# Kernel optimization log

Measured on AMD Instinct MI355X. Metric: run time of the kernel, lower is better.

Reference implementation:

```python
import jax, jax.numpy as jnp
import numpy as np

B = 32768; NF = 8; E = 16; V = 100000; D = 4
IN = 2 * NF * E          # 256 = id_dims + agn_dims
FCN = [256, 128, 64]
DIMS = [IN] + FCN
EPS = 1e-5               # BatchNorm1d eps


def setup_inputs() -> dict:
    ks = jax.random.split(jax.random.key(0), 64)
    inp = {
        'id_idx': jax.random.randint(ks[0], (B, NF), 0, V),
        'agn_idx': jax.random.randint(ks[1], (B, NF), 0, V),
        'domain_id': jax.random.randint(ks[2], (B,), 0, D),
        'id_tables': jax.random.normal(ks[3], (NF, V, E), dtype=jnp.float32) * 0.01,
        'agn_tables': jax.random.normal(ks[4], (NF, V, E), dtype=jnp.float32) * 0.01,
    }
    k = 5
    for i in range(len(FCN)):
        din, dout = DIMS[i], DIMS[i + 1]
        inp[f'mlp_W{i}'] = jax.random.normal(ks[k], (D, din, dout), dtype=jnp.float32) / np.sqrt(din).astype(np.float32); k += 1
        inp[f'mlp_b{i}'] = jnp.zeros((D, dout), jnp.float32)
        inp[f'bn_g{i}'] = jnp.ones((D, dout), jnp.float32)
        inp[f'bn_b{i}'] = jnp.zeros((D, dout), jnp.float32)
        inp[f'gate_W1_{i}'] = jax.random.normal(ks[k], (D, IN, dout), dtype=jnp.float32) / np.sqrt(IN).astype(np.float32); k += 1
        inp[f'gate_b1_{i}'] = jnp.zeros((D, dout), jnp.float32)
        inp[f'gate_W2_{i}'] = jax.random.normal(ks[k], (D, dout, dout), dtype=jnp.float32) / np.sqrt(dout).astype(np.float32); k += 1
        inp[f'gate_b2_{i}'] = jnp.zeros((D, dout), jnp.float32)
    inp['fin_W'] = jax.random.normal(ks[k], (D, DIMS[-1], 1), dtype=jnp.float32) / np.sqrt(DIMS[-1]).astype(np.float32)
    inp['fin_b'] = jnp.zeros((D, 1), jnp.float32)
    return inp


def _embed(tables, idx):
    # tables [NF,V,E], idx [B,NF] -> [B, NF*E] (per-feature lookup then concat)
    g = tables[jnp.arange(NF)[None, :], idx]            # [B,NF,E]
    return g.reshape(idx.shape[0], NF * E)


def _ppnet(id_tables, agn_tables, mlp_W, mlp_b, bn_g, bn_b, gW1, gb1, gW2, gb2,
           fin_W, fin_b, id_idx, agn_idx, domain_id):
    id_x = _embed(id_tables, id_idx)                    # [B, 128]
    agn_x = _embed(agn_tables, agn_idx)                 # [B, 128]
    # gate_input = cat(id_x, agn_x.detach())
    gate_in = jnp.concatenate([id_x, jax.lax.stop_gradient(agn_x)], axis=1)  # [B, IN]
    h = None
    for i in range(len(FCN)):
        # GateNU: Linear->ReLU->Linear->2*sigmoid, broadcast over D domain towers
        g1 = jax.nn.relu(jnp.einsum('bi,dio->dbo', gate_in, gW1[i]) + gb1[i][:, None, :])
        gate = 2.0 * jax.nn.sigmoid(jnp.einsum('dbo,dop->dbp', g1, gW2[i]) + gb2[i][:, None, :])
        # MLP layer: Linear -> BatchNorm1d (train-mode batch stats) -> ReLU
        if h is None:
            h = jnp.einsum('bi,dio->dbo', gate_in, mlp_W[i]) + mlp_b[i][:, None, :]
        else:
            h = jnp.einsum('dbi,dio->dbo', h, mlp_W[i]) + mlp_b[i][:, None, :]
        mu = h.mean(axis=1, keepdims=True)
        var = h.var(axis=1, keepdims=True)              # biased, matches torch BN training
        h = (h - mu) * jax.lax.rsqrt(var + EPS) * bn_g[i][:, None, :] + bn_b[i][:, None, :]
        h = jax.nn.relu(h)
        h = h * gate
    out = jax.nn.sigmoid(jnp.einsum('dbh,dho->dbo', h, fin_W) + fin_b[:, None, :])  # [D,B,1]
    out = out[:, :, 0]                                  # [D,B]
    # torch.where masked-select chain == gather the row of the assigned domain
    return out[domain_id, jnp.arange(out.shape[1])]     # [B]


def reference(id_idx, agn_idx, domain_id, id_tables, agn_tables,
              mlp_W0, mlp_b0, bn_g0, bn_b0, gate_W1_0, gate_b1_0, gate_W2_0, gate_b2_0,
              mlp_W1, mlp_b1, bn_g1, bn_b1, gate_W1_1, gate_b1_1, gate_W2_1, gate_b2_1,
              mlp_W2, mlp_b2, bn_g2, bn_b2, gate_W1_2, gate_b1_2, gate_W2_2, gate_b2_2,
              fin_W, fin_b):
    mlp_W = [mlp_W0, mlp_W1, mlp_W2]; mlp_b = [mlp_b0, mlp_b1, mlp_b2]
    bn_g = [bn_g0, bn_g1, bn_g2]; bn_b = [bn_b0, bn_b1, bn_b2]
    gW1 = [gate_W1_0, gate_W1_1, gate_W1_2]; gb1 = [gate_b1_0, gate_b1_1, gate_b1_2]
    gW2 = [gate_W2_0, gate_W2_1, gate_W2_2]; gb2 = [gate_b2_0, gate_b2_1, gate_b2_2]
    return _ppnet(id_tables, agn_tables, mlp_W, mlp_b, bn_g, bn_b, gW1, gb1, gW2, gb2,
                  fin_W, fin_b, id_idx, agn_idx, domain_id)
```

## Files before the change

### kernel.cpp

```cpp
#include <hip/hip_runtime.h>


typedef __attribute__((ext_vector_type(8))) short short8;
typedef __attribute__((ext_vector_type(4))) float floatx4;

#define BATCH 32768
#define NDOM 4
#define TM 64

__device__ __forceinline__ unsigned short f2b(float f) {
    unsigned u = __float_as_uint(f);
    u += 0x7fffu + ((u >> 16) & 1u);
    return (unsigned short)(u >> 16);
}
__device__ __forceinline__ float b2f(unsigned short h) {
    return __uint_as_float(((unsigned)h) << 16);
}

struct MatDesc { const float* src; unsigned K, N, pfx, total; };
struct PrepArgs { MatDesc m[9]; float* stats; unsigned statsN; unsigned grand; };

__global__ __launch_bounds__(256) void prep_k(PrepArgs a, unsigned short* __restrict__ wt) {
    unsigned e = blockIdx.x * 256 + threadIdx.x;
    if (e < a.statsN) a.stats[e] = 0.f;
    if (e >= a.grand) return;
    int j = 0;
    while (j < 8 && e >= a.m[j].pfx + a.m[j].total) j++;
    const unsigned K = a.m[j].K, N = a.m[j].N;
    const unsigned local = e - a.m[j].pfx;
    const unsigned kn = K * N;
    const unsigned d = local / kn;
    const unsigned r2 = local - d * kn;
    const unsigned n = r2 / K;
    const unsigned k = r2 - n * K;
    wt[e] = f2b(a.m[j].src[((long long)d * K + k) * N + n]);
}

__global__ __launch_bounds__(256) void embed_k(const int* __restrict__ idi, const int* __restrict__ agi,
                                               const float* __restrict__ idt, const float* __restrict__ agt,
                                               unsigned short* __restrict__ gin) {
    int t = blockIdx.x * 256 + threadIdx.x;
    int b = t >> 4, slot = t & 15;
    int f = slot & 7;
    const int* ip = (slot < 8) ? idi : agi;
    const float* tab = (slot < 8) ? idt : agt;
    int ix = ip[b * 8 + f];
    const float* src = tab + ((long long)f * 100000 + ix) * 16;
    unsigned short tmp[16];
#pragma unroll
    for (int j = 0; j < 16; j++) tmp[j] = f2b(src[j]);
    unsigned short* dst = gin + (long long)b * 256 + slot * 16;
    *(uint4*)dst = *(const uint4*)tmp;
    *(uint4*)(dst + 8) = *(const uint4*)(tmp + 8);
}

template <int N, int KX>
__global__ __launch_bounds__(256, 2) void stats_k(
    const unsigned short* __restrict__ X, int ginMode,
    const unsigned short* __restrict__ Wm,
    float* __restrict__ gsum, float* __restrict__ gssq) {
    constexpr int GX = KX / 8;
    constexpr int NW = N / 4, CT = NW / 16;
    __shared__ __align__(16) unsigned short tA[TM * KX];
    const int t = threadIdx.x;
    const int d = blockIdx.y;
    const int m0 = blockIdx.x * TM;
    const unsigned short* Xp = X + ((long long)(ginMode ? 0 : d * BATCH) + m0) * KX;
#pragma unroll
    for (int r = 0; r < TM * GX / 256; r++) {
        int idx = r * 256 + t;
        int m = idx / GX, j = idx % GX;
        uint4 v = *(const uint4*)(Xp + (long long)m * KX + j * 8);
        *(uint4*)&tA[(m * GX + (j ^ (m & 7))) * 8] = v;
    }
    __syncthreads();
    const int w = t >> 6, lane = t & 63, lrow = lane & 15, lq = lane >> 4;
    const int n0w = w * NW;
    const unsigned short* Wp = Wm + ((long long)d * N + n0w) * KX;
    floatx4 acc[4][CT];
#pragma unroll
    for (int rt = 0; rt < 4; rt++)
#pragma unroll
        for (int ct = 0; ct < CT; ct++) acc[rt][ct] = (floatx4)(0.f);
#pragma unroll
    for (int k0 = 0; k0 < KX; k0 += 32) {
        short8 a[4], b[CT];
#pragma unroll
        for (int rt = 0; rt < 4; rt++) {
            int m = rt * 16 + lrow;
            a[rt] = *(const short8*)&tA[(m * GX + (((k0 >> 3) | lq) ^ (m & 7))) * 8];
        }
#pragma unroll
        for (int ct = 0; ct < CT; ct++)
            b[ct] = *(const short8*)(Wp + (long long)(ct * 16 + lrow) * KX + k0 + lq * 8);
#pragma unroll
        for (int rt = 0; rt < 4; rt++)
#pragma unroll
            for (int ct = 0; ct < CT; ct++)
                acc[rt][ct] = __builtin_amdgcn_mfma_f32_16x16x32_bf16(a[rt], b[ct], acc[rt][ct], 0, 0, 0);
    }
#pragma unroll
    for (int ct = 0; ct < CT; ct++) {
        float s = 0.f, ss = 0.f;
#pragma unroll
        for (int rt = 0; rt < 4; rt++)
#pragma unroll
            for (int r = 0; r < 4; r++) { float v = acc[rt][ct][r]; s += v; ss += v * v; }
        s += __shfl_down(s, 32); ss += __shfl_down(ss, 32);
        s += __shfl_down(s, 16); ss += __shfl_down(ss, 16);
        if (lane < 16) {
            atomicAdd(&gsum[d * N + n0w + ct * 16 + lane], s);
            atomicAdd(&gssq[d * N + n0w + ct * 16 + lane], ss);
        }
    }
}

template <int N, int KX, bool SHARED_A, bool FINAL>
__global__ __launch_bounds__(256, 2) void fused_k(
    const unsigned short* __restrict__ gin,
    const unsigned short* __restrict__ Xh,
    const unsigned short* __restrict__ W1,
    const unsigned short* __restrict__ W2,
    const unsigned short* __restrict__ Wm,
    const float* __restrict__ gb1, const float* __restrict__ gb2,
    const float* __restrict__ gsum, const float* __restrict__ gssq,
    const float* __restrict__ gma, const float* __restrict__ bta, float invB,
    unsigned short* __restrict__ Xn,
    const int* __restrict__ dom, const float* __restrict__ fw,
    const float* __restrict__ fb, float* __restrict__ outp) {
    constexpr int GG = N / 8;
    constexpr int GX = KX / 8;
    constexpr int NW = N / 4, CT = NW / 16;
    constexpr int TXN = SHARED_A ? 8 : TM * KX;
    __shared__ __align__(16) unsigned short tG[TM * 256];
    __shared__ __align__(16) unsigned short tX[TXN];
    __shared__ __align__(16) unsigned short g1b[TM * N];
    const int t = threadIdx.x;
    const int d = blockIdx.y;
    const int m0 = blockIdx.x * TM;
    const int w = t >> 6, lane = t & 63, lrow = lane & 15, lq = lane >> 4;
    const int n0w = w * NW;

    {
        const unsigned short* Gp = gin + (long long)m0 * 256;
#pragma unroll
        for (int r = 0; r < 8; r++) {
            int idx = r * 256 + t;
            int m = idx >> 5, j = idx & 31;
            uint4 v = *(const uint4*)(Gp + (long long)m * 256 + j * 8);
            *(uint4*)&tG[((m << 5) + (j ^ (m & 7))) * 8] = v;
        }
    }
    if constexpr (!SHARED_A) {
        const unsigned short* Xp = Xh + ((long long)d * BATCH + m0) * KX;
#pragma unroll
        for (int r = 0; r < TM * GX / 256; r++) {
            int idx = r * 256 + t;
            int m = idx / GX, j = idx % GX;
            uint4 v = *(const uint4*)(Xp + (long long)m * KX + j * 8);
            *(uint4*)&tX[(m * GX + (j ^ (m & 7))) * 8] = v;
        }
    }
    __syncthreads();

    floatx4 acc1[4][CT], acch[4][CT];
#pragma unroll
    for (int rt = 0; rt < 4; rt++)
#pragma unroll
        for (int ct = 0; ct < CT; ct++) { acc1[rt][ct] = (floatx4)(0.f); acch[rt][ct] = (floatx4)(0.f); }
    const unsigned short* W1p = W1 + ((long long)d * N + n0w) * 256;
    const unsigned short* Wmp = Wm + ((long long)d * N + n0w) * KX;
#pragma unroll
    for (int k0 = 0; k0 < 256; k0 += 32) {
        short8 aG[4];
#pragma unroll
        for (int rt = 0; rt < 4; rt++) {
            int m = rt * 16 + lrow;
            aG[rt] = *(const short8*)&tG[((m << 5) + (((k0 >> 3) | lq) ^ (m & 7))) * 8];
        }
        short8 b1[CT];
#pragma unroll
        for (int ct = 0; ct < CT; ct++)
            b1[ct] = *(const short8*)(W1p + (long long)(ct * 16 + lrow) * 256 + k0 + lq * 8);
        if (k0 < KX) {
            short8 aX[4], bm[CT];
            if constexpr (SHARED_A) {
#pragma unroll
                for (int rt = 0; rt < 4; rt++) aX[rt] = aG[rt];
            } else {
#pragma unroll
                for (int rt = 0; rt < 4; rt++) {
                    int m = rt * 16 + lrow;
                    aX[rt] = *(const short8*)&tX[(m * GX + (((k0 >> 3) | lq) ^ (m & 7))) * 8];
                }
            }
#pragma unroll
            for (int ct = 0; ct < CT; ct++)
                bm[ct] = *(const short8*)(Wmp + (long long)(ct * 16 + lrow) * KX + k0 + lq * 8);
#pragma unroll
            for (int rt = 0; rt < 4; rt++)
#pragma unroll
                for (int ct = 0; ct < CT; ct++) {
                    acc1[rt][ct] = __builtin_amdgcn_mfma_f32_16x16x32_bf16(aG[rt], b1[ct], acc1[rt][ct], 0, 0, 0);
                    acch[rt][ct] = __builtin_amdgcn_mfma_f32_16x16x32_bf16(aX[rt], bm[ct], acch[rt][ct], 0, 0, 0);
                }
        } else {
#pragma unroll
            for (int rt = 0; rt < 4; rt++)
#pragma unroll
                for (int ct = 0; ct < CT; ct++)
                    acc1[rt][ct] = __builtin_amdgcn_mfma_f32_16x16x32_bf16(aG[rt], b1[ct], acc1[rt][ct], 0, 0, 0);
        }
    }
#pragma unroll
    for (int ct = 0; ct < CT; ct++) {
        int n = n0w + ct * 16 + lrow;
        float bs = gb1[d * N + n];
        int jj = n >> 3, sub = n & 7;
#pragma unroll
        for (int rt = 0; rt < 4; rt++)
#pragma unroll
            for (int r = 0; r < 4; r++) {
                int m = rt * 16 + lq * 4 + r;
                g1b[(m * GG + (jj ^ (m & 7))) * 8 + sub] = f2b(fmaxf(acc1[rt][ct][r] + bs, 0.f));
            }
    }
    __syncthreads();

    floatx4 acc2[4][CT];
#pragma unroll
    for (int rt = 0; rt < 4; rt++)
#pragma unroll
        for (int ct = 0; ct < CT; ct++) acc2[rt][ct] = (floatx4)(0.f);
    const unsigned short* W2p = W2 + ((long long)d * N + n0w) * N;
#pragma unroll
    for (int k0 = 0; k0 < N; k0 += 32) {
        short8 a[4], b[CT];
#pragma unroll
        for (int rt = 0; rt < 4; rt++) {
            int m = rt * 16 + lrow;
            a[rt] = *(const short8*)&g1b[(m * GG + (((k0 >> 3) | lq) ^ (m & 7))) * 8];
        }
#pragma unroll
        for (int ct = 0; ct < CT; ct++)
            b[ct] = *(const short8*)(W2p + (long long)(ct * 16 + lrow) * N + k0 + lq * 8);
#pragma unroll
        for (int rt = 0; rt < 4; rt++)
#pragma unroll
            for (int ct = 0; ct < CT; ct++)
                acc2[rt][ct] = __builtin_amdgcn_mfma_f32_16x16x32_bf16(a[rt], b[ct], acc2[rt][ct], 0, 0, 0);
    }
    __syncthreads();

#pragma unroll
    for (int ct = 0; ct < CT; ct++) {
        int n = n0w + ct * 16 + lrow;
        int i = d * N + n;
        float bs2 = gb2[i];
        float ma = gsum[i] * invB;
        float var = gssq[i] * invB - ma * ma;
        float sc = rsqrtf(var + 1e-5f) * gma[i];
        float sh = bta[i] - ma * sc;
        int jj = n >> 3, sub = n & 7;
#pragma unroll
        for (int rt = 0; rt < 4; rt++)
#pragma unroll
            for (int r = 0; r < 4; r++) {
                int m = rt * 16 + lq * 4 + r;
                float gate = 2.f / (1.f + __expf(-(acc2[rt][ct][r] + bs2)));
                float v = fmaxf(acch[rt][ct][r] * sc + sh, 0.f) * gate;
                g1b[(m * GG + (jj ^ (m & 7))) * 8 + sub] = f2b(v);
            }
    }
    __syncthreads();

    if (!FINAL) {
        unsigned short* Op = Xn + ((long long)d * BATCH + m0) * N;
#pragma unroll
        for (int r = 0; r < TM * GG / 256; r++) {
            int idx = r * 256 + t;
            int m = idx / GG, j = idx % GG;
            *(uint4*)(Op + (long long)m * N + j * 8) = *(const uint4*)&g1b[(m * GG + (j ^ (m & 7))) * 8];
        }
    } else {
        int m = t >> 2, q = t & 3;
        const float* fwp = fw + d * 64;
        float s = 0.f;
#pragma unroll
        for (int g = 0; g < 2; g++) {
            int j = q * 2 + g;
            short8 v = *(const short8*)&g1b[(m * 8 + (j ^ (m & 7))) * 8];
#pragma unroll
            for (int kk = 0; kk < 8; kk++)
                s += b2f((unsigned short)v[kk]) * fwp[j * 8 + kk];
        }
        s += __shfl_down(s, 1);
        s += __shfl_down(s, 2);
        if (q == 0) {
            int b = m0 + m;
            if (dom[b] == d) outp[b] = 1.f / (1.f + __expf(-(s + fb[d])));
        }
    }
}

extern "C" void kernel_launch(void* const* d_in, const int* in_sizes, int n_in,
                              void* d_out, int out_size, void* d_ws, size_t ws_size,
                              hipStream_t stream) {
    const int B = BATCH, D = NDOM;

    const int* id_idx = (const int*)d_in[0];
    const int* agn_idx = (const int*)d_in[1];
    const int* dom = (const int*)d_in[2];
    const float* id_t = (const float*)d_in[3];
    const float* agn_t = (const float*)d_in[4];
    const float *mlpW[3], *bng[3], *bnb[3], *gW1[3], *gb1[3], *gW2[3], *gb2[3];
    for (int i = 0; i < 3; i++) {
        int b0 = 5 + i * 8;
        mlpW[i] = (const float*)d_in[b0 + 0];
        bng[i] = (const float*)d_in[b0 + 2];
        bnb[i] = (const float*)d_in[b0 + 3];
        gW1[i] = (const float*)d_in[b0 + 4];
        gb1[i] = (const float*)d_in[b0 + 5];
        gW2[i] = (const float*)d_in[b0 + 6];
        gb2[i] = (const float*)d_in[b0 + 7];
    }
    const float* finW = (const float*)d_in[29];
    const float* finb = (const float*)d_in[30];

    char* wsc = (char*)d_ws;
    size_t off = 0;
    auto alloc = [&](size_t bytes) -> char* {
        char* p = wsc + off;
        off = (off + bytes + 255) & ~(size_t)255;
        return p;
    };

    struct { const float* src; int K, N; } mats[9] = {
        {mlpW[0], 256, 256}, {gW1[0], 256, 256}, {gW2[0], 256, 256},
        {mlpW[1], 256, 128}, {gW1[1], 256, 128}, {gW2[1], 128, 128},
        {mlpW[2], 128, 64},  {gW1[2], 256, 64},  {gW2[2], 64, 64}};
    unsigned pfx[10];
    pfx[0] = 0;
    for (int j = 0; j < 9; j++) pfx[j + 1] = pfx[j] + 4u * mats[j].K * mats[j].N;

    unsigned short* wt = (unsigned short*)alloc((size_t)pfx[9] * 2);
    unsigned short* gin = (unsigned short*)alloc((size_t)B * 256 * 2);
    float* stats = (float*)alloc((size_t)3 * 2 * D * 256 * 4);
    unsigned short* X1 = (unsigned short*)alloc((size_t)D * B * 256 * 2);
    unsigned short* X2 = (unsigned short*)alloc((size_t)D * B * 128 * 2);

    PrepArgs pa;
    for (int j = 0; j < 9; j++) {
        pa.m[j].src = mats[j].src;
        pa.m[j].K = (unsigned)mats[j].K;
        pa.m[j].N = (unsigned)mats[j].N;
        pa.m[j].pfx = pfx[j];
        pa.m[j].total = 4u * mats[j].K * mats[j].N;
    }
    pa.stats = stats;
    pa.statsN = 3 * 2 * D * 256;
    pa.grand = pfx[9];

    const float invB = 1.f / (float)B;
    dim3 gs(B / TM, D);

    prep_k<<<dim3((pfx[9] + 255) / 256), 256, 0, stream>>>(pa, wt);
    embed_k<<<dim3(B * 16 / 256), 256, 0, stream>>>(id_idx, agn_idx, id_t, agn_t, gin);

    float* gsum0 = stats + 0 * 2 * D * 256; float* gssq0 = gsum0 + D * 256;
    float* gsum1 = stats + 1 * 2 * D * 256; float* gssq1 = gsum1 + D * 256;
    float* gsum2 = stats + 2 * 2 * D * 256; float* gssq2 = gsum2 + D * 256;

    stats_k<256, 256><<<gs, 256, 0, stream>>>(gin, 1, wt + pfx[0], gsum0, gssq0);
    fused_k<256, 256, true, false><<<gs, 256, 0, stream>>>(
        gin, gin, wt + pfx[1], wt + pfx[2], wt + pfx[0], gb1[0], gb2[0],
        gsum0, gssq0, bng[0], bnb[0], invB,
        X1, nullptr, nullptr, nullptr, nullptr);

    stats_k<128, 256><<<gs, 256, 0, stream>>>(X1, 0, wt + pfx[3], gsum1, gssq1);
    fused_k<128, 256, false, false><<<gs, 256, 0, stream>>>(
        gin, X1, wt + pfx[4], wt + pfx[5], wt + pfx[3], gb1[1], gb2[1],
        gsum1, gssq1, bng[1], bnb[1], invB,
        X2, nullptr, nullptr, nullptr, nullptr);

    stats_k<64, 128><<<gs, 256, 0, stream>>>(X2, 0, wt + pfx[6], gsum2, gssq2);
    fused_k<64, 128, false, true><<<gs, 256, 0, stream>>>(
        gin, X2, wt + pfx[7], wt + pfx[8], wt + pfx[6], gb1[2], gb2[2],
        gsum2, gssq2, bng[2], bnb[2], invB,
        nullptr, dom, finW, finb, (float*)d_out);
}
```

Measured before the change: 535.2 us.

## Store pre-BN layer outputs and fuse next-layer matmul with stats into layer kernel

The separate stats kernels are removed, along with the recomputation of the pre-BN main-path matmul in the fused kernel. h0_k computes the first pre-BN activations, accumulates their BN statistics and writes them to memory. Each fused2_k then applies gating and BN to the stored h, computes the next layer's pre-BN matmul, accumulates its statistics and stores it. This cuts the kernel count from seven to five and drops the duplicate GEMMs. The cost is writing and reading bf16 pre-BN tensors through global memory, and shared memory is reused as a single buffer with extra barriers.

```diff
diff --git a/kernel.cpp b/kernel.cpp
--- a/kernel.cpp
+++ b/kernel.cpp
@@ -54,53 +54,52 @@
     *(uint4*)(dst + 8) = *(const uint4*)(tmp + 8);
 }
 
-template <int N, int KX>
-__global__ __launch_bounds__(256, 2) void stats_k(
-    const unsigned short* __restrict__ X, int ginMode,
+__global__ __launch_bounds__(256, 2) void h0_k(
+    const unsigned short* __restrict__ gin,
     const unsigned short* __restrict__ Wm,
-    float* __restrict__ gsum, float* __restrict__ gssq) {
-    constexpr int GX = KX / 8;
-    constexpr int NW = N / 4, CT = NW / 16;
-    __shared__ __align__(16) unsigned short tA[TM * KX];
+    float* __restrict__ gsum, float* __restrict__ gssq,
+    unsigned short* __restrict__ hOut) {
+    __shared__ __align__(16) unsigned short tA[TM * 256];
     const int t = threadIdx.x;
     const int d = blockIdx.y;
     const int m0 = blockIdx.x * TM;
-    const unsigned short* Xp = X + ((long long)(ginMode ? 0 : d * BATCH) + m0) * KX;
-#pragma unroll
-    for (int r = 0; r < TM * GX / 256; r++) {
+    const unsigned short* Xp = gin + (long long)m0 * 256;
+#pragma unroll
+    for (int r = 0; r < 8; r++) {
         int idx = r * 256 + t;
-        int m = idx / GX, j = idx % GX;
-        uint4 v = *(const uint4*)(Xp + (long long)m * KX + j * 8);
-        *(uint4*)&tA[(m * GX + (j ^ (m & 7))) * 8] = v;
+        int m = idx >> 5, j = idx & 31;
+        uint4 v = *(const uint4*)(Xp + (long long)m * 256 + j * 8);
+        *(uint4*)&tA[((m << 5) + (j ^ (m & 7))) * 8] = v;
     }
     __syncthreads();
     const int w = t >> 6, lane = t & 63, lrow = lane & 15, lq = lane >> 4;
-    const int n0w = w * NW;
-    const unsigned short* Wp = Wm + ((long long)d * N + n0w) * KX;
-    floatx4 acc[4][CT];
+    const int n0w = w * 64;
+    const unsigned short* Wp = Wm + ((long long)d * 256 + n0w) * 256;
+    floatx4 acc[4][4];
 #pragma unroll
     for (int rt = 0; rt < 4; rt++)
 #pragma unroll
-        for (int ct = 0; ct < CT; ct++) acc[rt][ct] = (floatx4)(0.f);
-#pragma unroll
-    for (int k0 = 0; k0 < KX; k0 += 32) {
-        short8 a[4], b[CT];
+        for (int ct = 0; ct < 4; ct++) acc[rt][ct] = (floatx4)(0.f);
+#pragma unroll
+    for (int k0 = 0; k0 < 256; k0 += 32) {
+        short8 a[4], b[4];
 #pragma unroll
         for (int rt = 0; rt < 4; rt++) {
             int m = rt * 16 + lrow;
-            a[rt] = *(const short8*)&tA[(m * GX + (((k0 >> 3) | lq) ^ (m & 7))) * 8];
-        }
-#pragma unroll
-        for (int ct = 0; ct < CT; ct++)
-            b[ct] = *(const short8*)(Wp + (long long)(ct * 16 + lrow) * KX + k0 + lq * 8);
-#pragma unroll
-        for (int rt = 0; rt < 4; rt++)
-#pragma unroll
-            for (int ct = 0; ct < CT; ct++)
+            a[rt] = *(const short8*)&tA[((m << 5) + (((k0 >> 3) | lq) ^ (m & 7))) * 8];
+        }
+#pragma unroll
+        for (int ct = 0; ct < 4; ct++)
+            b[ct] = *(const short8*)(Wp + (long long)(ct * 16 + lrow) * 256 + k0 + lq * 8);
+#pragma unroll
+        for (int rt = 0; rt < 4; rt++)
+#pragma unroll
+            for (int ct = 0; ct < 4; ct++)
                 acc[rt][ct] = __builtin_amdgcn_mfma_f32_16x16x32_bf16(a[rt], b[ct], acc[rt][ct], 0, 0, 0);
     }
-#pragma unroll
-    for (int ct = 0; ct < CT; ct++) {
+    __syncthreads();
+#pragma unroll
+    for (int ct = 0; ct < 4; ct++) {
         float s = 0.f, ss = 0.f;
 #pragma unroll
         for (int rt = 0; rt < 4; rt++)
@@ -109,32 +108,48 @@
         s += __shfl_down(s, 32); ss += __shfl_down(ss, 32);
         s += __shfl_down(s, 16); ss += __shfl_down(ss, 16);
         if (lane < 16) {
-            atomicAdd(&gsum[d * N + n0w + ct * 16 + lane], s);
-            atomicAdd(&gssq[d * N + n0w + ct * 16 + lane], ss);
-        }
-    }
-}
-
-template <int N, int KX, bool SHARED_A, bool FINAL>
-__global__ __launch_bounds__(256, 2) void fused_k(
+            atomicAdd(&gsum[d * 256 + n0w + ct * 16 + lane], s);
+            atomicAdd(&gssq[d * 256 + n0w + ct * 16 + lane], ss);
+        }
+        int n = n0w + ct * 16 + lrow;
+        int jj = n >> 3, sub = n & 7;
+#pragma unroll
+        for (int rt = 0; rt < 4; rt++)
+#pragma unroll
+            for (int r = 0; r < 4; r++) {
+                int m = rt * 16 + lq * 4 + r;
+                tA[((m << 5) + (jj ^ (m & 7))) * 8 + sub] = f2b(acc[rt][ct][r]);
+            }
+    }
+    __syncthreads();
+    unsigned short* Op = hOut + ((long long)d * BATCH + m0) * 256;
+#pragma unroll
+    for (int r = 0; r < 8; r++) {
+        int idx = r * 256 + t;
+        int m = idx >> 5, j = idx & 31;
+        *(uint4*)(Op + (long long)m * 256 + j * 8) = *(const uint4*)&tA[((m << 5) + (j ^ (m & 7))) * 8];
+    }
+}
+
+template <int N, int NH, bool FINAL>
+__global__ __launch_bounds__(256, 2) void fused2_k(
     const unsigned short* __restrict__ gin,
-    const unsigned short* __restrict__ Xh,
+    const unsigned short* __restrict__ hIn,
     const unsigned short* __restrict__ W1,
     const unsigned short* __restrict__ W2,
-    const unsigned short* __restrict__ Wm,
+    const unsigned short* __restrict__ WmN,
     const float* __restrict__ gb1, const float* __restrict__ gb2,
     const float* __restrict__ gsum, const float* __restrict__ gssq,
     const float* __restrict__ gma, const float* __restrict__ bta, float invB,
-    unsigned short* __restrict__ Xn,
+    unsigned short* __restrict__ hNext,
+    float* __restrict__ gsumN, float* __restrict__ gssqN,
     const int* __restrict__ dom, const float* __restrict__ fw,
     const float* __restrict__ fb, float* __restrict__ outp) {
     constexpr int GG = N / 8;
-    constexpr int GX = KX / 8;
     constexpr int NW = N / 4, CT = NW / 16;
-    constexpr int TXN = SHARED_A ? 8 : TM * KX;
-    __shared__ __align__(16) unsigned short tG[TM * 256];
-    __shared__ __align__(16) unsigned short tX[TXN];
-    __shared__ __align__(16) unsigned short g1b[TM * N];
+    constexpr int NWH = NH / 4, CTH = NH / 64;
+    constexpr int GH = NH / 8;
+    __shared__ __align__(16) unsigned short buf[TM * 256];
     const int t = threadIdx.x;
     const int d = blockIdx.y;
     const int m0 = blockIdx.x * TM;
@@ -148,70 +163,36 @@
             int idx = r * 256 + t;
             int m = idx >> 5, j = idx & 31;
             uint4 v = *(const uint4*)(Gp + (long long)m * 256 + j * 8);
-            *(uint4*)&tG[((m << 5) + (j ^ (m & 7))) * 8] = v;
-        }
-    }
-    if constexpr (!SHARED_A) {
-        const unsigned short* Xp = Xh + ((long long)d * BATCH + m0) * KX;
-#pragma unroll
-        for (int r = 0; r < TM * GX / 256; r++) {
-            int idx = r * 256 + t;
-            int m = idx / GX, j = idx % GX;
-            uint4 v = *(const uint4*)(Xp + (long long)m * KX + j * 8);
-            *(uint4*)&tX[(m * GX + (j ^ (m & 7))) * 8] = v;
-        }
-    }
-    __syncthreads();
-
-    floatx4 acc1[4][CT], acch[4][CT];
+            *(uint4*)&buf[((m << 5) + (j ^ (m & 7))) * 8] = v;
+        }
+    }
+    __syncthreads();
+
+    floatx4 acc1[4][CT];
 #pragma unroll
     for (int rt = 0; rt < 4; rt++)
 #pragma unroll
-        for (int ct = 0; ct < CT; ct++) { acc1[rt][ct] = (floatx4)(0.f); acch[rt][ct] = (floatx4)(0.f); }
+        for (int ct = 0; ct < CT; ct++) acc1[rt][ct] = (floatx4)(0.f);
     const unsigned short* W1p = W1 + ((long long)d * N + n0w) * 256;
-    const unsigned short* Wmp = Wm + ((long long)d * N + n0w) * KX;
 #pragma unroll
     for (int k0 = 0; k0 < 256; k0 += 32) {
-        short8 aG[4];
+        short8 a[4], b[CT];
 #pragma unroll
         for (int rt = 0; rt < 4; rt++) {
             int m = rt * 16 + lrow;
-            aG[rt] = *(const short8*)&tG[((m << 5) + (((k0 >> 3) | lq) ^ (m & 7))) * 8];
-        }
-        short8 b1[CT];
+            a[rt] = *(const short8*)&buf[((m << 5) + (((k0 >> 3) | lq) ^ (m & 7))) * 8];
+        }
 #pragma unroll
         for (int ct = 0; ct < CT; ct++)
-            b1[ct] = *(const short8*)(W1p + (long long)(ct * 16 + lrow) * 256 + k0 + lq * 8);
-        if (k0 < KX) {
-            short8 aX[4], bm[CT];
-            if constexpr (SHARED_A) {
-#pragma unroll
-                for (int rt = 0; rt < 4; rt++) aX[rt] = aG[rt];
-            } else {
-#pragma unroll
-                for (int rt = 0; rt < 4; rt++) {
-                    int m = rt * 16 + lrow;
-                    aX[rt] = *(const short8*)&tX[(m * GX + (((k0 >> 3) | lq) ^ (m & 7))) * 8];
-                }
-            }
+            b[ct] = *(const short8*)(W1p + (long long)(ct * 16 + lrow) * 256 + k0 + lq * 8);
+#pragma unroll
+        for (int rt = 0; rt < 4; rt++)
 #pragma unroll
             for (int ct = 0; ct < CT; ct++)
-                bm[ct] = *(const short8*)(Wmp + (long long)(ct * 16 + lrow) * KX + k0 + lq * 8);
-#pragma unroll
-            for (int rt = 0; rt < 4; rt++)
-#pragma unroll
-                for (int ct = 0; ct < CT; ct++) {
-                    acc1[rt][ct] = __builtin_amdgcn_mfma_f32_16x16x32_bf16(aG[rt], b1[ct], acc1[rt][ct], 0, 0, 0);
-                    acch[rt][ct] = __builtin_amdgcn_mfma_f32_16x16x32_bf16(aX[rt], bm[ct], acch[rt][ct], 0, 0, 0);
-                }
-        } else {
-#pragma unroll
-            for (int rt = 0; rt < 4; rt++)
-#pragma unroll
-                for (int ct = 0; ct < CT; ct++)
-                    acc1[rt][ct] = __builtin_amdgcn_mfma_f32_16x16x32_bf16(aG[rt], b1[ct], acc1[rt][ct], 0, 0, 0);
-        }
-    }
+                acc1[rt][ct] = __builtin_amdgcn_mfma_f32_16x16x32_bf16(a[rt], b[ct], acc1[rt][ct], 0, 0, 0);
+    }
+    __syncthreads();
+
 #pragma unroll
     for (int ct = 0; ct < CT; ct++) {
         int n = n0w + ct * 16 + lrow;
@@ -222,7 +203,7 @@
 #pragma unroll
             for (int r = 0; r < 4; r++) {
                 int m = rt * 16 + lq * 4 + r;
-                g1b[(m * GG + (jj ^ (m & 7))) * 8 + sub] = f2b(fmaxf(acc1[rt][ct][r] + bs, 0.f));
+                buf[(m * GG + (jj ^ (m & 7))) * 8 + sub] = f2b(fmaxf(acc1[rt][ct][r] + bs, 0.f));
             }
     }
     __syncthreads();
@@ -239,7 +220,7 @@
 #pragma unroll
         for (int rt = 0; rt < 4; rt++) {
             int m = rt * 16 + lrow;
-            a[rt] = *(const short8*)&g1b[(m * GG + (((k0 >> 3) | lq) ^ (m & 7))) * 8];
+            a[rt] = *(const short8*)&buf[(m * GG + (((k0 >> 3) | lq) ^ (m & 7))) * 8];
         }
 #pragma unroll
         for (int ct = 0; ct < CT; ct++)
@@ -249,6 +230,28 @@
 #pragma unroll
             for (int ct = 0; ct < CT; ct++)
                 acc2[rt][ct] = __builtin_amdgcn_mfma_f32_16x16x32_bf16(a[rt], b[ct], acc2[rt][ct], 0, 0, 0);
+    }
+    float gate[4][CT][4];
+#pragma unroll
+    for (int ct = 0; ct < CT; ct++) {
+        float bs2 = gb2[d * N + n0w + ct * 16 + lrow];
+#pragma unroll
+        for (int rt = 0; rt < 4; rt++)
+#pragma unroll
+            for (int r = 0; r < 4; r++)
+                gate[rt][ct][r] = 2.f / (1.f + __expf(-(acc2[rt][ct][r] + bs2)));
+    }
+    __syncthreads();
+
+    {
+        const unsigned short* Hp = hIn + ((long long)d * BATCH + m0) * N;
+#pragma unroll
+        for (int r = 0; r < TM * GG / 256; r++) {
+            int idx = r * 256 + t;
+            int m = idx / GG, j = idx % GG;
+            uint4 v = *(const uint4*)(Hp + (long long)m * N + j * 8);
+            *(uint4*)&buf[(m * GG + (j ^ (m & 7))) * 8] = v;
+        }
     }
     __syncthreads();
 
@@ -256,7 +259,6 @@
     for (int ct = 0; ct < CT; ct++) {
         int n = n0w + ct * 16 + lrow;
         int i = d * N + n;
-        float bs2 = gb2[i];
         float ma = gsum[i] * invB;
         float var = gssq[i] * invB - ma * ma;
         float sc = rsqrtf(var + 1e-5f) * gma[i];
@@ -267,20 +269,69 @@
 #pragma unroll
             for (int r = 0; r < 4; r++) {
                 int m = rt * 16 + lq * 4 + r;
-                float gate = 2.f / (1.f + __expf(-(acc2[rt][ct][r] + bs2)));
-                float v = fmaxf(acch[rt][ct][r] * sc + sh, 0.f) * gate;
-                g1b[(m * GG + (jj ^ (m & 7))) * 8 + sub] = f2b(v);
+                int idx = (m * GG + (jj ^ (m & 7))) * 8 + sub;
+                float hv = b2f(buf[idx]);
+                buf[idx] = f2b(fmaxf(hv * sc + sh, 0.f) * gate[rt][ct][r]);
             }
     }
     __syncthreads();
 
-    if (!FINAL) {
-        unsigned short* Op = Xn + ((long long)d * BATCH + m0) * N;
-#pragma unroll
-        for (int r = 0; r < TM * GG / 256; r++) {
+    if constexpr (!FINAL) {
+        const int n0h = w * NWH;
+        floatx4 acch[4][CTH];
+#pragma unroll
+        for (int rt = 0; rt < 4; rt++)
+#pragma unroll
+            for (int ct = 0; ct < CTH; ct++) acch[rt][ct] = (floatx4)(0.f);
+        const unsigned short* Wp = WmN + ((long long)d * NH + n0h) * N;
+#pragma unroll
+        for (int k0 = 0; k0 < N; k0 += 32) {
+            short8 a[4], b[CTH];
+#pragma unroll
+            for (int rt = 0; rt < 4; rt++) {
+                int m = rt * 16 + lrow;
+                a[rt] = *(const short8*)&buf[(m * GG + (((k0 >> 3) | lq) ^ (m & 7))) * 8];
+            }
+#pragma unroll
+            for (int ct = 0; ct < CTH; ct++)
+                b[ct] = *(const short8*)(Wp + (long long)(ct * 16 + lrow) * N + k0 + lq * 8);
+#pragma unroll
+            for (int rt = 0; rt < 4; rt++)
+#pragma unroll
+                for (int ct = 0; ct < CTH; ct++)
+                    acch[rt][ct] = __builtin_amdgcn_mfma_f32_16x16x32_bf16(a[rt], b[ct], acch[rt][ct], 0, 0, 0);
+        }
+        __syncthreads();
+#pragma unroll
+        for (int ct = 0; ct < CTH; ct++) {
+            float s = 0.f, ss = 0.f;
+#pragma unroll
+            for (int rt = 0; rt < 4; rt++)
+#pragma unroll
+                for (int r = 0; r < 4; r++) { float v = acch[rt][ct][r]; s += v; ss += v * v; }
+            s += __shfl_down(s, 32); ss += __shfl_down(ss, 32);
+            s += __shfl_down(s, 16); ss += __shfl_down(ss, 16);
+            if (lane < 16) {
+                atomicAdd(&gsumN[d * NH + n0h + ct * 16 + lane], s);
+                atomicAdd(&gssqN[d * NH + n0h + ct * 16 + lane], ss);
+            }
+            int n = n0h + ct * 16 + lrow;
+            int jj = n >> 3, sub = n & 7;
+#pragma unroll
+            for (int rt = 0; rt < 4; rt++)
+#pragma unroll
+                for (int r = 0; r < 4; r++) {
+                    int m = rt * 16 + lq * 4 + r;
+                    buf[(m * GH + (jj ^ (m & 7))) * 8 + sub] = f2b(acch[rt][ct][r]);
+                }
+        }
+        __syncthreads();
+        unsigned short* Op = hNext + ((long long)d * BATCH + m0) * NH;
+#pragma unroll
+        for (int r = 0; r < TM * GH / 256; r++) {
             int idx = r * 256 + t;
-            int m = idx / GG, j = idx % GG;
-            *(uint4*)(Op + (long long)m * N + j * 8) = *(const uint4*)&g1b[(m * GG + (j ^ (m & 7))) * 8];
+            int m = idx / GH, j = idx % GH;
+            *(uint4*)(Op + (long long)m * NH + j * 8) = *(const uint4*)&buf[(m * GH + (j ^ (m & 7))) * 8];
         }
     } else {
         int m = t >> 2, q = t & 3;
@@ -289,7 +340,7 @@
 #pragma unroll
         for (int g = 0; g < 2; g++) {
             int j = q * 2 + g;
-            short8 v = *(const short8*)&g1b[(m * 8 + (j ^ (m & 7))) * 8];
+            short8 v = *(const short8*)&buf[(m * 8 + (j ^ (m & 7))) * 8];
 #pragma unroll
             for (int kk = 0; kk < 8; kk++)
                 s += b2f((unsigned short)v[kk]) * fwp[j * 8 + kk];
@@ -346,8 +397,9 @@
     unsigned short* wt = (unsigned short*)alloc((size_t)pfx[9] * 2);
     unsigned short* gin = (unsigned short*)alloc((size_t)B * 256 * 2);
     float* stats = (float*)alloc((size_t)3 * 2 * D * 256 * 4);
-    unsigned short* X1 = (unsigned short*)alloc((size_t)D * B * 256 * 2);
-    unsigned short* X2 = (unsigned short*)alloc((size_t)D * B * 128 * 2);
+    unsigned short* h0 = (unsigned short*)alloc((size_t)D * B * 256 * 2);
+    unsigned short* h1 = (unsigned short*)alloc((size_t)D * B * 128 * 2);
+    unsigned short* h2 = h0;
 
     PrepArgs pa;
     for (int j = 0; j < 9; j++) {
@@ -371,21 +423,20 @@
     float* gsum1 = stats + 1 * 2 * D * 256; float* gssq1 = gsum1 + D * 256;
     float* gsum2 = stats + 2 * 2 * D * 256; float* gssq2 = gsum2 + D * 256;
 
-    stats_k<256, 256><<<gs, 256, 0, stream>>>(gin, 1, wt + pfx[0], gsum0, gssq0);
-    fused_k<256, 256, true, false><<<gs, 256, 0, stream>>>(
-        gin, gin, wt + pfx[1], wt + pfx[2], wt + pfx[0], gb1[0], gb2[0],
+    h0_k<<<gs, 256, 0, stream>>>(gin, wt + pfx[0], gsum0, gssq0, h0);
+
+    fused2_k<256, 128, false><<<gs, 256, 0, stream>>>(
+        gin, h0, wt + pfx[1], wt + pfx[2], wt + pfx[3], gb1[0], gb2[0],
         gsum0, gssq0, bng[0], bnb[0], invB,
-        X1, nullptr, nullptr, nullptr, nullptr);
-
-    stats_k<128, 256><<<gs, 256, 0, stream>>>(X1, 0, wt + pfx[3], gsum1, gssq1);
-    fused_k<128, 256, false, false><<<gs, 256, 0, stream>>>(
-        gin, X1, wt + pfx[4], wt + pfx[5], wt + pfx[3], gb1[1], gb2[1],
+        h1, gsum1, gssq1, nullptr, nullptr, nullptr, nullptr);
+
+    fused2_k<128, 64, false><<<gs, 256, 0, stream>>>(
+        gin, h1, wt + pfx[4], wt + pfx[5], wt + pfx[6], gb1[1], gb2[1],
         gsum1, gssq1, bng[1], bnb[1], invB,
-        X2, nullptr, nullptr, nullptr, nullptr);
-
-    stats_k<64, 128><<<gs, 256, 0, stream>>>(X2, 0, wt + pfx[6], gsum2, gssq2);
-    fused_k<64, 128, false, true><<<gs, 256, 0, stream>>>(
-        gin, X2, wt + pfx[7], wt + pfx[8], wt + pfx[6], gb1[2], gb2[2],
+        h2, gsum2, gssq2, nullptr, nullptr, nullptr, nullptr);
+
+    fused2_k<64, 64, true><<<gs, 256, 0, stream>>>(
+        gin, h2, wt + pfx[7], wt + pfx[8], nullptr, gb1[2], gb2[2],
         gsum2, gssq2, bng[2], bnb[2], invB,
-        nullptr, dom, finW, finb, (float*)d_out);
-}
+        nullptr, nullptr, nullptr, dom, finW, finb, (float*)d_out);
+}
```

Measured after the change: 470.4 us. 1.14x faster.
